# Kernel optimization log

Hardware: AMD Instinct MI355X
Metric: run time of the kernel (lower is better)

Reference implementation:

```python
import jax, jax.numpy as jnp
import numpy as np

N = 4096
STD = 0.01


def setup_inputs() -> dict:
    key = jax.random.key(0)
    ks = jax.random.split(key, 16)
    p = lambda k, shape: STD * jax.random.normal(k, shape, dtype=jnp.float32)
    return {
        "t": 0,
        "x": jax.random.normal(ks[0], (N, 1), dtype=jnp.float32),
        "A": jax.random.normal(ks[1], (N, N), dtype=jnp.float32),
        # MLP_A: 2 -> 16 -> 16 -> 1 (ReLU between hidden layers), torch (out,in) layout
        "WA0": p(ks[2], (16, 2)), "bA0": p(ks[3], (16,)),
        "WA1": p(ks[4], (16, 16)), "bA1": p(ks[5], (16,)),
        "WA2": p(ks[6], (1, 16)), "bA2": p(ks[7], (1,)),
        # MLP: 1 -> 16 -> 1 (ReLU after first layer)
        "Wm0": p(ks[8], (16, 1)), "bm0": p(ks[9], (16,)),
        "Wm1": p(ks[10], (1, 16)), "bm1": p(ks[11], (1,)),
        # linear_A: 2 -> 1, no bias; linear_f: 1 -> 1, no bias
        "wA": p(ks[12], (1, 2)),
        "wf": p(ks[13], (1, 1)),
    }


def reference(t, x, A, WA0, bA0, WA1, bA1, WA2, bA2, Wm0, bm0, Wm1, bm1, wA, wf):
    n = x.shape[0]
    # node MLP branch: hidden_list[0] == 1 != 0
    x_N = jax.nn.relu(x @ Wm0.T + bm0) @ Wm1.T + bm1 + x @ wf.T  # (n, 1)
    # all-pairs features: x_a[i, j] = (x_i, x_j)
    x1 = jnp.broadcast_to(x, (n, n))       # row i = x_i repeated
    x2 = jnp.broadcast_to(x.T, (n, n))     # row i = full x vector
    x_a = jnp.stack((x1, x2), axis=-1)     # (n, n, 2)
    # edge MLP (2 -> 16 -> 16 -> 1) + skip linear_A (2 -> 1)
    h = jax.nn.relu(x_a @ WA0.T + bA0)     # (n, n, 16)
    h = jax.nn.relu(h @ WA1.T + bA1)       # (n, n, 16)
    x_e = (h @ WA2.T + bA2)[..., 0]        # (n, n)
    x_12 = (x_a @ wA.T)[..., 0]            # (n, n)
    # adjacency-weighted reduction over neighbors (dim=1)
    x_A = jnp.sum(A * (x_e + x_12), axis=1, keepdims=True)  # (n, 1)
    return x_N + x_A
```

## Files before the change

kernel.cpp:

```cpp
#include <hip/hip_runtime.h>
#include <hip/hip_bf16.h>


#define NN 4096

typedef __fp16 half8  __attribute__((ext_vector_type(8)));
typedef __fp16 half2v __attribute__((ext_vector_type(2)));
typedef __attribute__((ext_vector_type(4)))  float f32x4;
typedef __attribute__((ext_vector_type(16))) float f32x16;

__device__ __forceinline__ half2v cvt2(float lo, float hi) {
    return __builtin_amdgcn_cvt_pkrtz(lo, hi);
}

__global__ __launch_bounds__(256, 4) void odef_kernel(
    const float* __restrict__ x,  const float* __restrict__ A,
    const float* __restrict__ WA0, const float* __restrict__ bA0,
    const float* __restrict__ WA1, const float* __restrict__ bA1,
    const float* __restrict__ WA2, const float* __restrict__ bA2,
    const float* __restrict__ Wm0, const float* __restrict__ bm0,
    const float* __restrict__ Wm1, const float* __restrict__ bm1,
    const float* __restrict__ wA,  const float* __restrict__ wf,
    float* __restrict__ out)
{
    __shared__ float partial[4];

    const int tid  = threadIdx.x;
    const int wave = tid >> 6;
    const int lane = tid & 63;
    const int n    = lane & 31;
    const int half = lane >> 5;
    const int row  = blockIdx.x * 2 + (wave >> 1);
    const int jbase = (wave & 1) * (NN / 2);

    const float xi = x[row];

    union { half2v h2[4]; half8 h8; } au;
    #pragma unroll
    for (int p = 0; p < 4; ++p) {
        float lo = 0.f, hi = 0.f;
        if (n < 16) {
            int k = half * 8 + p * 2;
            lo = WA1[n * 16 + k];
            hi = WA1[n * 16 + k + 1];
        }
        au.h2[p] = cvt2(lo, hi);
    }

    half2v u2h[4], w2h[4];
    #pragma unroll
    for (int p = 0; p < 4; ++p) {
        int k0 = half * 8 + p * 2;
        u2h[p] = cvt2(fmaf(WA0[2 * k0],     xi, bA0[k0]),
                      fmaf(WA0[2 * k0 + 2], xi, bA0[k0 + 1]));
        w2h[p] = cvt2(WA0[2 * k0 + 1], WA0[2 * k0 + 3]);
    }

    float wa2s[8];
    f32x16 cbias;
    #pragma unroll
    for (int r = 0; r < 16; ++r) cbias[r] = 0.f;
    #pragma unroll
    for (int r = 0; r < 8; ++r) {
        int m = (r & 3) + 8 * (r >> 2) + 4 * half;
        wa2s[r]  = WA2[m];
        cbias[r] = bA1[m];
    }

    const float wA1h = half ? 0.f : wA[1];
    const float c0h  = half ? 0.f : (bA2[0] + wA[0] * xi);
    const half2v z2 = { (__fp16)0.f, (__fp16)0.f };

    const f32x4* xp4 = (const f32x4*)(x + jbase) + n;
    const f32x4* ap4 = (const f32x4*)(A + (size_t)row * NN + jbase) + n;

    float acc = 0.f;

    f32x4 xc = xp4[0];
    f32x4 ac = ap4[0];

    for (int it = 0; it < 16; ++it) {
        const f32x4* xnp = (it + 1 < 16) ? xp4 + 32 : xp4;
        const f32x4* anp = (it + 1 < 16) ? ap4 + 32 : ap4;
        f32x4 xN = xnp[0];
        f32x4 aN = anp[0];

        #pragma unroll
        for (int q = 0; q < 4; q += 2) {
            half2v xgh0 = cvt2(xc[q], xc[q]);
            union { half2v h2[4]; half8 h8; } b0;
            #pragma unroll
            for (int p = 0; p < 4; ++p)
                b0.h2[p] = __builtin_elementwise_max(w2h[p] * xgh0 + u2h[p], z2);
            f32x16 d0 = __builtin_amdgcn_mfma_f32_32x32x16_f16(au.h8, b0.h8, cbias, 0, 0, 0);

            half2v xgh1 = cvt2(xc[q + 1], xc[q + 1]);
            union { half2v h2[4]; half8 h8; } b1;
            #pragma unroll
            for (int p = 0; p < 4; ++p)
                b1.h2[p] = __builtin_elementwise_max(w2h[p] * xgh1 + u2h[p], z2);
            f32x16 d1 = __builtin_amdgcn_mfma_f32_32x32x16_f16(au.h8, b1.h8, cbias, 0, 0, 0);

            {
                float pp = fmaf(wA1h, xc[q], c0h);
                #pragma unroll
                for (int r = 0; r < 8; ++r)
                    pp = fmaf(wa2s[r], fmaxf(d0[r], 0.f), pp);
                acc = fmaf(ac[q], pp, acc);
            }
            {
                float pp = fmaf(wA1h, xc[q + 1], c0h);
                #pragma unroll
                for (int r = 0; r < 8; ++r)
                    pp = fmaf(wa2s[r], fmaxf(d1[r], 0.f), pp);
                acc = fmaf(ac[q + 1], pp, acc);
            }
        }
        xc = xN; ac = aN;
        xp4 = xnp; ap4 = anp;
    }

    #pragma unroll
    for (int off = 32; off > 0; off >>= 1)
        acc += __shfl_xor(acc, off);
    if (lane == 0) partial[wave] = acc;
    __syncthreads();

    if (lane == 0 && (wave & 1) == 0) {
        float xn = fmaf(wf[0], xi, bm1[0]);
        #pragma unroll
        for (int h = 0; h < 16; ++h)
            xn = fmaf(Wm1[h], fmaxf(fmaf(Wm0[h], xi, bm0[h]), 0.f), xn);
        out[row] = xn + partial[wave] + partial[wave + 1];
    }
}

extern "C" void kernel_launch(void* const* d_in, const int* in_sizes, int n_in,
                              void* d_out, int out_size, void* d_ws, size_t ws_size,
                              hipStream_t stream) {
    const float* x   = (const float*)d_in[1];
    const float* A   = (const float*)d_in[2];
    const float* WA0 = (const float*)d_in[3];
    const float* bA0 = (const float*)d_in[4];
    const float* WA1 = (const float*)d_in[5];
    const float* bA1 = (const float*)d_in[6];
    const float* WA2 = (const float*)d_in[7];
    const float* bA2 = (const float*)d_in[8];
    const float* Wm0 = (const float*)d_in[9];
    const float* bm0 = (const float*)d_in[10];
    const float* Wm1 = (const float*)d_in[11];
    const float* bm1 = (const float*)d_in[12];
    const float* wA  = (const float*)d_in[13];
    const float* wf  = (const float*)d_in[14];
    float* out = (float*)d_out;

    odef_kernel<<<NN / 2, 256, 0, stream>>>(x, A, WA0, bA0, WA1, bA1, WA2, bA2,
                                            Wm0, bm0, Wm1, bm1, wA, wf, out);
}
```

Before: 145.0 us.

## Move layer-2 epilogue to packed fp16 dot2 and raise occupancy target

Replaces the scalar fp32 epilogue (8 fmax plus 8 fma per output) with packed fp16 work: convert pairs of MFMA results, add the bias in half2, ReLU in half2, then a v_dot2 accumulate into fp32. The bias is no longer folded into the MFMA accumulator, so the MFMA starts from a zero constant. Launch bounds go from 4 to 6 waves per EU, the last loop iteration is peeled to drop the per-iteration pointer selects, and two accumulators are kept. Doing the layer-2 activations in fp16 loses precision, and the tighter register budget can cause spills.

```diff
diff --git a/kernel.cpp b/kernel.cpp
--- a/kernel.cpp
+++ b/kernel.cpp
@@ -13,7 +13,7 @@
     return __builtin_amdgcn_cvt_pkrtz(lo, hi);
 }
 
-__global__ __launch_bounds__(256, 4) void odef_kernel(
+__global__ __launch_bounds__(256, 6) void odef_kernel(
     const float* __restrict__ x,  const float* __restrict__ A,
     const float* __restrict__ WA0, const float* __restrict__ bA0,
     const float* __restrict__ WA1, const float* __restrict__ bA1,
@@ -56,70 +56,78 @@
         w2h[p] = cvt2(WA0[2 * k0 + 1], WA0[2 * k0 + 3]);
     }
 
-    float wa2s[8];
-    f32x16 cbias;
+    half2v wa2h[4], bb[4];
     #pragma unroll
-    for (int r = 0; r < 16; ++r) cbias[r] = 0.f;
-    #pragma unroll
-    for (int r = 0; r < 8; ++r) {
-        int m = (r & 3) + 8 * (r >> 2) + 4 * half;
-        wa2s[r]  = WA2[m];
-        cbias[r] = bA1[m];
+    for (int p = 0; p < 4; ++p) {
+        int r  = 2 * p;
+        int m0 = (r & 3) + 8 * (r >> 2) + 4 * half;
+        wa2h[p] = cvt2(WA2[m0], WA2[m0 + 1]);
+        bb[p]   = cvt2(bA1[m0], bA1[m0 + 1]);
     }
 
     const float wA1h = half ? 0.f : wA[1];
     const float c0h  = half ? 0.f : (bA2[0] + wA[0] * xi);
     const half2v z2 = { (__fp16)0.f, (__fp16)0.f };
+    const f32x16 zc = {};
 
     const f32x4* xp4 = (const f32x4*)(x + jbase) + n;
     const f32x4* ap4 = (const f32x4*)(A + (size_t)row * NN + jbase) + n;
 
-    float acc = 0.f;
+    float acc0 = 0.f, acc1 = 0.f;
 
     f32x4 xc = xp4[0];
     f32x4 ac = ap4[0];
 
-    for (int it = 0; it < 16; ++it) {
-        const f32x4* xnp = (it + 1 < 16) ? xp4 + 32 : xp4;
-        const f32x4* anp = (it + 1 < 16) ? ap4 + 32 : ap4;
-        f32x4 xN = xnp[0];
-        f32x4 aN = anp[0];
-
+    auto body = [&](const f32x4 xv, const f32x4 av) {
         #pragma unroll
         for (int q = 0; q < 4; q += 2) {
-            half2v xgh0 = cvt2(xc[q], xc[q]);
+            half2v xg0 = cvt2(xv[q], xv[q]);
             union { half2v h2[4]; half8 h8; } b0;
             #pragma unroll
             for (int p = 0; p < 4; ++p)
-                b0.h2[p] = __builtin_elementwise_max(w2h[p] * xgh0 + u2h[p], z2);
-            f32x16 d0 = __builtin_amdgcn_mfma_f32_32x32x16_f16(au.h8, b0.h8, cbias, 0, 0, 0);
+                b0.h2[p] = __builtin_elementwise_max(w2h[p] * xg0 + u2h[p], z2);
+            f32x16 d0 = __builtin_amdgcn_mfma_f32_32x32x16_f16(au.h8, b0.h8, zc, 0, 0, 0);
 
-            half2v xgh1 = cvt2(xc[q + 1], xc[q + 1]);
+            half2v xg1 = cvt2(xv[q + 1], xv[q + 1]);
             union { half2v h2[4]; half8 h8; } b1;
             #pragma unroll
             for (int p = 0; p < 4; ++p)
-                b1.h2[p] = __builtin_elementwise_max(w2h[p] * xgh1 + u2h[p], z2);
-            f32x16 d1 = __builtin_amdgcn_mfma_f32_32x32x16_f16(au.h8, b1.h8, cbias, 0, 0, 0);
+                b1.h2[p] = __builtin_elementwise_max(w2h[p] * xg1 + u2h[p], z2);
+            f32x16 d1 = __builtin_amdgcn_mfma_f32_32x32x16_f16(au.h8, b1.h8, zc, 0, 0, 0);
 
             {
-                float pp = fmaf(wA1h, xc[q], c0h);
+                float pp = fmaf(wA1h, xv[q], c0h);
                 #pragma unroll
-                for (int r = 0; r < 8; ++r)
-                    pp = fmaf(wa2s[r], fmaxf(d0[r], 0.f), pp);
-                acc = fmaf(ac[q], pp, acc);
+                for (int p = 0; p < 4; ++p) {
+                    half2v t = __builtin_elementwise_max(
+                        cvt2(d0[2 * p], d0[2 * p + 1]) + bb[p], z2);
+                    pp = __builtin_amdgcn_fdot2(t, wa2h[p], pp, false);
+                }
+                acc0 = fmaf(av[q], pp, acc0);
             }
             {
-                float pp = fmaf(wA1h, xc[q + 1], c0h);
+                float pp = fmaf(wA1h, xv[q + 1], c0h);
                 #pragma unroll
-                for (int r = 0; r < 8; ++r)
-                    pp = fmaf(wa2s[r], fmaxf(d1[r], 0.f), pp);
-                acc = fmaf(ac[q + 1], pp, acc);
+                for (int p = 0; p < 4; ++p) {
+                    half2v t = __builtin_elementwise_max(
+                        cvt2(d1[2 * p], d1[2 * p + 1]) + bb[p], z2);
+                    pp = __builtin_amdgcn_fdot2(t, wa2h[p], pp, false);
+                }
+                acc1 = fmaf(av[q + 1], pp, acc1);
             }
         }
+    };
+
+    for (int it = 0; it < 15; ++it) {
+        f32x4 xN = xp4[32];
+        f32x4 aN = ap4[32];
+        xp4 += 32; ap4 += 32;
+        body(xc, ac);
         xc = xN; ac = aN;
-        xp4 = xnp; ap4 = anp;
     }
+    body(xc, ac);
 
+    float acc = acc0 + acc1;
     #pragma unroll
     for (int off = 32; off > 0; off >>= 1)
         acc += __shfl_xor(acc, off);
```

New measurement: 144.1 us. About the same (-0.6%).
